# Performance work log

Hardware: AMD Instinct MI355X
Metric: run time of the kernel (lower is better)

## Reference

```python
import jax, jax.numpy as jnp
import numpy as np

L, B, T, C, H, D, F, W = 2, 2, 2048, 1024, 16, 64, 4096, 256
NEG = -1e9
EPS = 1e-6


def _rms(x, g):
    return x * jax.lax.rsqrt(jnp.mean(x * x, axis=-1, keepdims=True) + EPS) * g


def setup_inputs() -> dict:
    key = jax.random.key(0)
    ks = jax.random.split(key, 12)
    s = 0.02
    return {
        "x": jax.random.normal(ks[0], (B, T, C), jnp.float32),
        "retrieval_context": jax.random.normal(ks[1], (B, C), jnp.float32),
        "norm1_g": jnp.ones((L, C), jnp.float32),
        "Wqkv": jax.random.normal(ks[2], (L, C, 3 * C), jnp.float32) * s,
        "Wproj": jax.random.normal(ks[3], (L, C, C), jnp.float32) * s,
        "gate_W": jax.random.normal(ks[4], (L, C, 3), jnp.float32) * 0.01,
        "gate_b": jnp.zeros((L, 3), jnp.float32),
        "ret_W": jax.random.normal(ks[5], (L, C, C), jnp.float32) * 0.01,
        "norm2_g": jnp.ones((L, C), jnp.float32),
        "ffn_gate_W": jax.random.normal(ks[6], (L, C, F), jnp.float32) * s,
        "ffn_up_W": jax.random.normal(ks[7], (L, C, F), jnp.float32) * s,
        "ffn_down_W": jax.random.normal(ks[8], (L, F, C), jnp.float32) * s,
    }


def reference(x, retrieval_context, norm1_g, Wqkv, Wproj, gate_W, gate_b, ret_W,
              norm2_g, ffn_gate_W, ffn_up_W, ffn_down_W):
    # Sliding-window causal mask: key j visible to query i iff i-W+1 <= j <= i
    pos = jnp.arange(T)
    allowed = (pos[None, :] <= pos[:, None]) & (pos[None, :] >= pos[:, None] - W + 1)
    mask = jnp.where(allowed, 0.0, NEG).astype(x.dtype)  # (T, T)
    scale = 1.0 / np.sqrt(D)

    for l in range(L):
        h = _rms(x, norm1_g[l])                              # (B,T,C)
        qkv = h @ Wqkv[l]                                    # (B,T,3C)
        q, k, v = jnp.split(qkv, 3, axis=-1)
        q = q.reshape(B, T, H, D).transpose(0, 2, 1, 3)       # (B,H,T,D)
        k = k.reshape(B, T, H, D).transpose(0, 2, 1, 3)
        v = v.reshape(B, T, H, D).transpose(0, 2, 1, 3)
        scores = jnp.einsum("bhqd,bhkd->bhqk", q, k) * scale + mask
        attn = jax.nn.softmax(scores, axis=-1)
        o = jnp.einsum("bhqk,bhkd->bhqd", attn, v)
        attn_out = o.transpose(0, 2, 1, 3).reshape(B, T, C) @ Wproj[l]

        # TRN disabled: trn_out == 0, gate channel 1 pinned to -1e9
        gate_logits = h @ gate_W[l] + gate_b[l]               # (B,T,3)
        gate_logits = gate_logits.at[..., 1].set(NEG)
        gates = jax.nn.softmax(gate_logits, axis=-1)

        ret_out = (retrieval_context @ ret_W[l])[:, None, :]   # (B,1,C) broadcast over T
        mixed = gates[..., 0:1] * attn_out + gates[..., 2:3] * ret_out
        x = x + mixed

        h2 = _rms(x, norm2_g[l])
        ffn = (jax.nn.silu(h2 @ ffn_gate_W[l]) * (h2 @ ffn_up_W[l])) @ ffn_down_W[l]
        x = x + ffn
    return x
```

## Files before the change

### kernel.cpp

```cpp
#include <hip/hip_runtime.h>

#define L_ 2
#define B_ 2
#define T_ 2048
#define C_ 1024
#define H_ 16
#define D_ 64
#define F_ 4096
#define NTOK 4096
#define NELEM 4194304

typedef unsigned short u16;
typedef __attribute__((ext_vector_type(8))) short short8;
typedef __attribute__((ext_vector_type(4))) float float4v;

__device__ __forceinline__ float bf2f(u16 u) {
  unsigned v = ((unsigned)u) << 16;
  return __builtin_bit_cast(float, v);
}
__device__ __forceinline__ u16 f2bf(float f) {
  unsigned u = __builtin_bit_cast(unsigned, f);
  u += 0x7FFFu + ((u >> 16) & 1u);
  return (u16)(u >> 16);
}

__global__ void k_copyf(const float* __restrict__ in, float* __restrict__ out) {
  const int i = blockIdx.x * 256 + threadIdx.x;
  out[i] = in[i];
}

__device__ __forceinline__ void rms_tail(float* vloc, const float* __restrict__ g,
                                         u16* __restrict__ orow) {
  float s = vloc[0] * vloc[0] + vloc[1] * vloc[1] + vloc[2] * vloc[2] + vloc[3] * vloc[3];
#pragma unroll
  for (int o = 32; o; o >>= 1) s += __shfl_down(s, o);
  __shared__ float red[4];
  __shared__ float rsv;
  if ((threadIdx.x & 63) == 0) red[threadIdx.x >> 6] = s;
  __syncthreads();
  if (threadIdx.x == 0) {
    float t = red[0] + red[1] + red[2] + red[3];
    rsv = rsqrtf(t * (1.f / C_) + 1e-6f);
  }
  __syncthreads();
  const float rr = rsv;
#pragma unroll
  for (int i = 0; i < 4; i++) {
    const int c = threadIdx.x + i * 256;
    orow[c] = f2bf(vloc[i] * rr * g[c]);
  }
}

__global__ __launch_bounds__(256) void k_rms_first(const float* __restrict__ xin,
                                                   const float* __restrict__ g,
                                                   float* __restrict__ x,
                                                   u16* __restrict__ out) {
  const int row = blockIdx.x;
  const float* sr = xin + (size_t)row * C_;
  float* xr = x + (size_t)row * C_;
  float vloc[4];
#pragma unroll
  for (int i = 0; i < 4; i++) {
    const int c = threadIdx.x + i * 256;
    const float v = sr[c];
    vloc[i] = v;
    xr[c] = v;
  }
  rms_tail(vloc, g, out + (size_t)row * C_);
}

__global__ __launch_bounds__(256) void k_rms(const float* __restrict__ x,
                                             const float* __restrict__ g,
                                             u16* __restrict__ out) {
  const int row = blockIdx.x;
  const float* xr = x + (size_t)row * C_;
  float vloc[4];
#pragma unroll
  for (int i = 0; i < 4; i++) vloc[i] = xr[threadIdx.x + i * 256];
  rms_tail(vloc, g, out + (size_t)row * C_);
}

__global__ __launch_bounds__(256) void k_rms2mix(float* __restrict__ x,
                                                 const float* __restrict__ gates,
                                                 const float* __restrict__ ret,
                                                 const float* __restrict__ g,
                                                 u16* __restrict__ out) {
  const int row = blockIdx.x;
  const int b = row >> 11;
  const float g2 = gates[row * 2 + 1];
  const float* rr_ = ret + b * C_;
  float* xr = x + (size_t)row * C_;
  float vloc[4];
#pragma unroll
  for (int i = 0; i < 4; i++) {
    const int c = threadIdx.x + i * 256;
    const float v = xr[c] + g2 * rr_[c];
    vloc[i] = v;
    xr[c] = v;
  }
  rms_tail(vloc, g, out + (size_t)row * C_);
}

__global__ void k_tr2(const float* __restrict__ s0, u16* __restrict__ d0,
                      int K0, int N0, int t0,
                      const float* __restrict__ s1, u16* __restrict__ d1,
                      int K1, int N1) {
  __shared__ float tile[32][33];
  int t = blockIdx.x;
  const float* src; u16* dst; int K, N;
  if (t < t0) { src = s0; dst = d0; K = K0; N = N0; }
  else { t -= t0; src = s1; dst = d1; K = K1; N = N1; }
  const int ntx = N >> 5;
  const int tx = t % ntx, ty = t / ntx;
  const int x = tx * 32 + threadIdx.x;
  const int y0 = ty * 32 + threadIdx.y;
#pragma unroll
  for (int i = 0; i < 32; i += 8) tile[threadIdx.y + i][threadIdx.x] = src[(size_t)(y0 + i) * N + x];
  __syncthreads();
  const int x2 = ty * 32 + threadIdx.x;
  const int y2 = tx * 32 + threadIdx.y;
#pragma unroll
  for (int i = 0; i < 32; i += 8) dst[(size_t)(y2 + i) * K + x2] = f2bf(tile[threadIdx.x][threadIdx.y + i]);
}

__global__ void k_tr1(const float* __restrict__ in, u16* __restrict__ out, int K, int N) {
  __shared__ float tile[32][33];
  const int ntx = N >> 5;
  const int tx = blockIdx.x % ntx, ty = blockIdx.x / ntx;
  const int x = tx * 32 + threadIdx.x;
  const int y0 = ty * 32 + threadIdx.y;
#pragma unroll
  for (int i = 0; i < 32; i += 8) tile[threadIdx.y + i][threadIdx.x] = in[(size_t)(y0 + i) * N + x];
  __syncthreads();
  const int x2 = ty * 32 + threadIdx.x;
  const int y2 = tx * 32 + threadIdx.y;
#pragma unroll
  for (int i = 0; i < 32; i += 8) out[(size_t)(y2 + i) * K + x2] = f2bf(tile[threadIdx.x][threadIdx.y + i]);
}

__global__ void k_vt(const u16* __restrict__ qkv, u16* __restrict__ Vt) {
  __shared__ u16 tile[32][34];
  const int jt = blockIdx.x;
  const int dt = blockIdx.y;
  const int bh = blockIdx.z;
  const int b = bh >> 4;
  const int h = bh & 15;
  const int tx = threadIdx.x, ty = threadIdx.y;
#pragma unroll
  for (int i = 0; i < 32; i += 8) {
    const int j = jt * 32 + ty + i;
    const int d = dt * 32 + tx;
    tile[ty + i][tx] = qkv[(size_t)(b * T_ + j) * (3 * C_) + 2 * C_ + h * D_ + d];
  }
  __syncthreads();
#pragma unroll
  for (int i = 0; i < 32; i += 8) {
    const int d = dt * 32 + ty + i;
    const int j = jt * 32 + tx;
    Vt[(size_t)(bh * D_ + d) * T_ + j] = tile[tx][ty + i];
  }
}


#define VMW(n) asm volatile("s_waitcnt vmcnt(" #n ")" ::: "memory")
#define LGKM0 asm volatile("s_waitcnt lgkmcnt(0)" ::: "memory")
#define GBAR() __builtin_amdgcn_s_barrier()
#define PRIO1() __builtin_amdgcn_s_setprio(1)
#define PRIO0() __builtin_amdgcn_s_setprio(0)

#define STG8(gsrc, grow0, dstbyte, kk)                                                    \
  do {                                                                                    \
    const u16* g0_ = (gsrc) + (size_t)((grow0) + wid * 8 + srow) * K + (kk) + scol;       \
    __builtin_amdgcn_global_load_lds(                                                     \
        (const __attribute__((address_space(1))) void*)g0_,                               \
        (__attribute__((address_space(3))) void*)(lc + (dstbyte) + wid * 8 * 128),        \
        16, 0, 0);                                                                        \
    const u16* g1_ = g0_ + (size_t)64 * K;                                                \
    __builtin_amdgcn_global_load_lds(                                                     \
        (const __attribute__((address_space(1))) void*)g1_,                               \
        (__attribute__((address_space(3))) void*)(lc + (dstbyte) + (64 + wid * 8) * 128), \
        16, 0, 0);                                                                        \
  } while (0)

#define RDA4(dst, bufbyte, ig0)                                                           \
  { _Pragma("unroll") for (int i_ = 0; i_ < 4; ++i_) {                                    \
      _Pragma("unroll") for (int s_ = 0; s_ < 2; ++s_)                                    \
        dst[i_][s_] = *(const short8*)(lc + (bufbyte) +                                   \
            (wm * 128 + ((ig0) + i_) * 16 + m16) * 128 + (((s_ * 4 + quad) ^ csw) * 16)); } }

#define RDB4(dst, bufbyte, jg0)                                                           \
  { _Pragma("unroll") for (int j_ = 0; j_ < 2; ++j_) {                                    \
      _Pragma("unroll") for (int s_ = 0; s_ < 2; ++s_)                                    \
        dst[j_][s_] = *(const short8*)(lc + (bufbyte) +                                   \
            (wn * 64 + ((jg0) + j_) * 16 + m16) * 128 + (((s_ * 4 + quad) ^ csw) * 16)); } }

#define RDBS(dst, bufbyte)                                                                \
  { _Pragma("unroll") for (int j_ = 0; j_ < 2; ++j_) {                                    \
      _Pragma("unroll") for (int s_ = 0; s_ < 2; ++s_)                                    \
        dst[j_][s_] = *(const short8*)(lc + (bufbyte) +                                   \
            (wn * 32 + j_ * 16 + m16) * 128 + (((s_ * 4 + quad) ^ csw) * 16)); } }

#define MM16(ig0, jg0, bv_)                                                               \
  { _Pragma("unroll") for (int i_ = 0; i_ < 4; ++i_) {                                    \
      _Pragma("unroll") for (int j_ = 0; j_ < 2; ++j_) {                                  \
        _Pragma("unroll") for (int s_ = 0; s_ < 2; ++s_)                                  \
          acc[(ig0) + i_][(jg0) + j_] = __builtin_amdgcn_mfma_f32_16x16x32_bf16(          \
              av[i_][s_], bv_[j_][s_], acc[(ig0) + i_][(jg0) + j_], 0, 0, 0); } } }

#define MMS(accv, ig0, bv_)                                                               \
  { _Pragma("unroll") for (int i_ = 0; i_ < 4; ++i_) {                                    \
      _Pragma("unroll") for (int j_ = 0; j_ < 2; ++j_) {                                  \
        _Pragma("unroll") for (int s_ = 0; s_ < 2; ++s_)                                  \
          accv[(ig0) + i_][j_] = __builtin_amdgcn_mfma_f32_16x16x32_bf16(                 \
              av[i_][s_], bv_[j_][s_], accv[(ig0) + i_][j_], 0, 0, 0); } } }

template <int EPI>
__global__ __launch_bounds__(512, 2) void k_g256(const u16* __restrict__ A,
                                                 const u16* __restrict__ Bt,
                                                 u16* __restrict__ Cc,
                                                 float* __restrict__ Xf,
                                                 const float* __restrict__ gates,
                                                 int N, int K) {
  extern __shared__ __align__(16) u16 lds[];
  char* const lc = (char*)lds;
  enum { A0B = 0, B0B = 32768, A1B = 65536, B1B = 98304 };
  const int tid = threadIdx.x;
  const int wid = tid >> 6, lane = tid & 63;
  const int wm = wid >> 2, wn = wid & 3;
  const int quad = lane >> 4, m16 = lane & 15;
  const int srow = lane >> 3, sc = lane & 7;
  const int scol = ((sc ^ srow) & 7) * 8;
  const int csw = m16 & 7;
  const int m0 = blockIdx.x * 256, n0 = blockIdx.y * 256;
  const int Kslice = K / gridDim.z;
  const int kbeg = blockIdx.z * Kslice;
  const int ntile = Kslice >> 6;
  const int nit = ntile >> 1;

  float4v acc[8][4];
#pragma unroll
  for (int i = 0; i < 8; i++)
#pragma unroll
    for (int j = 0; j < 4; j++) acc[i][j] = (float4v){0.f, 0.f, 0.f, 0.f};
  short8 av[4][2], b01[2][2], b23[2][2];

  STG8(Bt, n0, B0B, kbeg);
  STG8(Bt, n0 + 128, B0B + 16384, kbeg);
  STG8(A, m0, A0B, kbeg);
  STG8(A, m0 + 128, A0B + 16384, kbeg);
  STG8(Bt, n0, B1B, kbeg + 64);
  STG8(Bt, n0 + 128, B1B + 16384, kbeg + 64);
  VMW(4);
  GBAR();

#pragma unroll 1
  for (int it = 0; it < nit; ++it) {
    const int t2 = 2 * it + 2, t3 = 2 * it + 3;
    const int k1 = kbeg + (2 * it + 1) * 64;
    const int k2 = kbeg + (t2 < ntile ? t2 : t2 - ntile) * 64;
    const int k3 = kbeg + (t3 < ntile ? t3 : t3 - ntile) * 64;
    RDA4(av, A0B, 0);
    RDB4(b01, B0B, 0);
    STG8(A, m0, A1B, k1);
    GBAR(); LGKM0;
    PRIO1(); MM16(0, 0, b01); PRIO0();
    GBAR();
    RDB4(b23, B0B, 2);
    STG8(A, m0 + 128, A1B + 16384, k1);
    GBAR(); LGKM0;
    PRIO1(); MM16(0, 2, b23); PRIO0();
    GBAR();
    RDA4(av, A0B, 4);
    STG8(Bt, n0, B0B, k2);
    GBAR(); LGKM0;
    PRIO1(); MM16(4, 2, b23); PRIO0();
    GBAR();
    STG8(Bt, n0 + 128, B0B + 16384, k2);
    VMW(4);
    GBAR(); LGKM0;
    PRIO1(); MM16(4, 0, b01); PRIO0();
    GBAR();
    RDA4(av, A1B, 0);
    RDB4(b01, B1B, 0);
    STG8(A, m0, A0B, k2);
    GBAR(); LGKM0;
    PRIO1(); MM16(0, 0, b01); PRIO0();
    GBAR();
    RDB4(b23, B1B, 2);
    STG8(A, m0 + 128, A0B + 16384, k2);
    GBAR(); LGKM0;
    PRIO1(); MM16(0, 2, b23); PRIO0();
    GBAR();
    RDA4(av, A1B, 4);
    STG8(Bt, n0, B1B, k3);
    GBAR(); LGKM0;
    PRIO1(); MM16(4, 2, b23); PRIO0();
    GBAR();
    STG8(Bt, n0 + 128, B1B + 16384, k3);
    VMW(4);
    GBAR(); LGKM0;
    PRIO1(); MM16(4, 0, b01); PRIO0();
    GBAR();
  }

#pragma unroll
  for (int i = 0; i < 8; i++) {
    const int row0 = m0 + wm * 128 + i * 16 + quad * 4;
#pragma unroll
    for (int j = 0; j < 4; j++) {
      const int col = n0 + wn * 64 + j * 16 + m16;
#pragma unroll
      for (int r = 0; r < 4; r++) {
        const size_t idx = (size_t)(row0 + r) * N + col;
        const float v = acc[i][j][r];
        if (EPI == 0) Cc[idx] = f2bf(v);
        else if (EPI == 1) unsafeAtomicAdd(&Xf[idx], gates[(row0 + r) * 2] * v);
        else unsafeAtomicAdd(&Xf[idx], v);
      }
    }
  }
}

__global__ __launch_bounds__(512, 2) void k_g256s(const u16* __restrict__ A,
                                                  const u16* __restrict__ Btg,
                                                  const u16* __restrict__ Btu,
                                                  u16* __restrict__ Cc,
                                                  int N, int K) {
  extern __shared__ __align__(16) u16 lds[];
  char* const lc = (char*)lds;
  enum { SA0 = 0, SG0 = 32768, SU0 = 49152, SA1 = 65536, SG1 = 98304, SU1 = 114688 };
  const int tid = threadIdx.x;
  const int wid = tid >> 6, lane = tid & 63;
  const int wm = wid >> 2, wn = wid & 3;
  const int quad = lane >> 4, m16 = lane & 15;
  const int srow = lane >> 3, sc = lane & 7;
  const int scol = ((sc ^ srow) & 7) * 8;
  const int csw = m16 & 7;
  const int m0 = blockIdx.x * 256, n0 = blockIdx.y * 128;
  const int kbeg = 0;
  const int ntile = K >> 6;
  const int nit = ntile >> 1;

  float4v accg[8][2], accu[8][2];
#pragma unroll
  for (int i = 0; i < 8; i++)
#pragma unroll
    for (int j = 0; j < 2; j++) {
      accg[i][j] = (float4v){0.f, 0.f, 0.f, 0.f};
      accu[i][j] = (float4v){0.f, 0.f, 0.f, 0.f};
    }
  short8 av[4][2], bg[2][2], bu[2][2];

  STG8(Btg, n0, SG0, kbeg);
  STG8(Btu, n0, SU0, kbeg);
  STG8(A, m0, SA0, kbeg);
  STG8(A, m0 + 128, SA0 + 16384, kbeg);
  STG8(Btg, n0, SG1, kbeg + 64);
  STG8(Btu, n0, SU1, kbeg + 64);
  STG8(A, m0, SA1, kbeg + 64);
  VMW(6);
  GBAR();

#pragma unroll 1
  for (int it = 0; it < nit; ++it) {
    const int t2 = 2 * it + 2, t3 = 2 * it + 3;
    const int k1 = kbeg + (2 * it + 1) * 64;
    const int k2 = kbeg + (t2 < ntile ? t2 : t2 - ntile) * 64;
    const int k3 = kbeg + (t3 < ntile ? t3 : t3 - ntile) * 64;
    RDA4(av, SA0, 0);
    RDBS(bg, SG0);
    STG8(A, m0 + 128, SA1 + 16384, k1);
    GBAR(); LGKM0;
    PRIO1(); MMS(accg, 0, bg); PRIO0();
    GBAR();
    RDBS(bu, SU0);
    STG8(Btg, n0, SG0, k2);
    GBAR(); LGKM0;
    PRIO1(); MMS(accu, 0, bu); PRIO0();
    GBAR();
    RDA4(av, SA0, 4);
    STG8(Btu, n0, SU0, k2);
    GBAR(); LGKM0;
    PRIO1(); MMS(accu, 4, bu); PRIO0();
    GBAR();
    STG8(A, m0, SA0, k2);
    VMW(6);
    GBAR(); LGKM0;
    PRIO1(); MMS(accg, 4, bg); PRIO0();
    GBAR();
    RDA4(av, SA1, 0);
    RDBS(bg, SG1);
    STG8(A, m0 + 128, SA0 + 16384, k2);
    GBAR(); LGKM0;
    PRIO1(); MMS(accg, 0, bg); PRIO0();
    GBAR();
    RDBS(bu, SU1);
    STG8(Btg, n0, SG1, k3);
    GBAR(); LGKM0;
    PRIO1(); MMS(accu, 0, bu); PRIO0();
    GBAR();
    RDA4(av, SA1, 4);
    STG8(Btu, n0, SU1, k3);
    GBAR(); LGKM0;
    PRIO1(); MMS(accu, 4, bu); PRIO0();
    GBAR();
    STG8(A, m0, SA1, k3);
    VMW(6);
    GBAR(); LGKM0;
    PRIO1(); MMS(accg, 4, bg); PRIO0();
    GBAR();
  }

#pragma unroll
  for (int i = 0; i < 8; i++) {
    const int row0 = m0 + wm * 128 + i * 16 + quad * 4;
#pragma unroll
    for (int j = 0; j < 2; j++) {
      const int col = n0 + wn * 32 + j * 16 + m16;
#pragma unroll
      for (int r = 0; r < 4; r++) {
        const float g = accg[i][j][r];
        const float u = accu[i][j][r];
        Cc[(size_t)(row0 + r) * N + col] = f2bf(u * g / (1.f + __expf(-g)));
      }
    }
  }
}

__global__ __launch_bounds__(256) void k_attn(const u16* __restrict__ qkv,
                                              const u16* __restrict__ Vt,
                                              u16* __restrict__ o) {
  __shared__ u16 lds[4][16][290];
  const int wave = threadIdx.x >> 6;
  const int widG = blockIdx.x * 4 + wave;
  const int lane = threadIdx.x & 63;
  const int quad = lane >> 4;
  const int c16 = lane & 15;
  const int qt = (widG & 127) * 16;
  const int h = (widG >> 7) & 15;
  const int b = widG >> 11;
  const size_t rs = 3 * C_;
  const int jt0 = qt - 256;

  const u16* qrow = qkv + (size_t)(b * T_ + qt + c16) * rs + h * D_ + quad * 8;
  const short8 a0 = *(const short8*)(qrow);
  const short8 a1 = *(const short8*)(qrow + 32);
  float4v S[17];
  const short8 z8 = (short8){0, 0, 0, 0, 0, 0, 0, 0};
#pragma unroll
  for (int t = 0; t < 17; t++) {
    if (jt0 + t * 16 + 15 < 0) { S[t] = (float4v){0.f, 0.f, 0.f, 0.f}; continue; }
    const int j = jt0 + t * 16 + c16;
    short8 b0 = z8, b1 = z8;
    if (j >= 0) {
      const u16* krow = qkv + (size_t)(b * T_ + j) * rs + C_ + h * D_ + quad * 8;
      b0 = *(const short8*)(krow);
      b1 = *(const short8*)(krow + 32);
    }
    float4v z = (float4v){0.f, 0.f, 0.f, 0.f};
    z = __builtin_amdgcn_mfma_f32_16x16x32_bf16(a0, b0, z, 0, 0, 0);
    z = __builtin_amdgcn_mfma_f32_16x16x32_bf16(a1, b1, z, 0, 0, 0);
    S[t] = z;
  }
#pragma unroll
  for (int r = 0; r < 4; r++) {
    const int q = qt + quad * 4 + r;
    float mx = -1.0e30f;
#pragma unroll
    for (int t = 0; t < 17; t++) {
      const int j = jt0 + t * 16 + c16;
      const int w = j - q + 255;
      const bool vis = (j >= 0) && (w >= 0) && (w < 256);
      if (vis) {
        const float s = S[t][r] * 0.125f;
        S[t][r] = s;
        mx = fmaxf(mx, s);
      } else {
        S[t][r] = -1.0e30f;
      }
    }
#pragma unroll
    for (int o2 = 1; o2 < 16; o2 <<= 1) mx = fmaxf(mx, __shfl_xor(mx, o2));
    float sum = 0.f;
#pragma unroll
    for (int t = 0; t < 17; t++) {
      const float e = (S[t][r] > -0.9e30f) ? __expf(S[t][r] - mx) : 0.f;
      S[t][r] = e;
      sum += e;
    }
#pragma unroll
    for (int o2 = 1; o2 < 16; o2 <<= 1) sum += __shfl_xor(sum, o2);
    const float inv = 1.f / fmaxf(sum, 1e-30f);
    const int prow = quad * 4 + r;
#pragma unroll
    for (int t = 0; t < 17; t++) lds[wave][prow][t * 16 + c16] = f2bf(S[t][r] * inv);
    lds[wave][prow][272 + c16] = 0;
  }
  __syncthreads();

  float4v acc[4];
#pragma unroll
  for (int md = 0; md < 4; md++) acc[md] = (float4v){0.f, 0.f, 0.f, 0.f};
  const u16* vtb = Vt + (size_t)((b * H_ + h) * D_) * T_;
  const uint* prow32 = (const uint*)(&lds[wave][c16][0]);
  union { short8 s8; uint u[4]; } bf;
#pragma unroll
  for (int c = 0; c < 9; c++) {
    const int jbase = jt0 + c * 32;
    if (jbase + 31 < 0) continue;
#pragma unroll
    for (int w2 = 0; w2 < 4; w2++) bf.u[w2] = prow32[c * 16 + quad * 4 + w2];
    int j0 = jbase + quad * 8;
    j0 = (j0 < 0) ? 0 : ((j0 > T_ - 8) ? (T_ - 8) : j0);
#pragma unroll
    for (int md = 0; md < 4; md++) {
      const short8 af = *(const short8*)(vtb + (size_t)(md * 16 + c16) * T_ + j0);
      acc[md] = __builtin_amdgcn_mfma_f32_16x16x32_bf16(af, bf.s8, acc[md], 0, 0, 0);
    }
  }
#pragma unroll
  for (int md = 0; md < 4; md++) {
    uint u0 = (uint)f2bf(acc[md][0]) | ((uint)f2bf(acc[md][1]) << 16);
    uint u1 = (uint)f2bf(acc[md][2]) | ((uint)f2bf(acc[md][3]) << 16);
    uint2 pk = make_uint2(u0, u1);
    u16* dst = o + (size_t)(b * T_ + qt + c16) * C_ + h * D_ + md * 16 + quad * 4;
    *(uint2*)dst = pk;
  }
}

__global__ __launch_bounds__(256) void k_gate(const u16* __restrict__ h,
                                              const float* __restrict__ gW,
                                              const float* __restrict__ gb,
                                              float* __restrict__ gates) {
  const int row = blockIdx.x * 4 + (threadIdx.x >> 6);
  const int lane = threadIdx.x & 63;
  const u16* hr = h + (size_t)row * C_;
  float s0 = 0.f, s2 = 0.f;
  for (int k = lane; k < C_; k += 64) {
    const float hv = bf2f(hr[k]);
    s0 += hv * gW[k * 3 + 0];
    s2 += hv * gW[k * 3 + 2];
  }
#pragma unroll
  for (int o = 32; o; o >>= 1) { s0 += __shfl_down(s0, o); s2 += __shfl_down(s2, o); }
  if (lane == 0) {
    const float l0 = s0 + gb[0];
    const float l2 = s2 + gb[2];
    const float m = fmaxf(l0, l2);
    const float e0 = __expf(l0 - m), e2 = __expf(l2 - m);
    const float inv = 1.f / (e0 + e2);
    gates[row * 2 + 0] = e0 * inv;
    gates[row * 2 + 1] = e2 * inv;
  }
}

__global__ void k_ret2(const float* __restrict__ rc, const float* __restrict__ rW,
                       float* __restrict__ ret) {
  const int l = blockIdx.x >> 3;
  const int bid = blockIdx.x & 7;
  const int b = bid >> 2;
  const int col = (bid & 3) * 256 + threadIdx.x;
  const float* rWl = rW + (size_t)l * C_ * C_;
  float s = 0.f;
  for (int k = 0; k < C_; k++) s += rc[b * C_ + k] * rWl[(size_t)k * C_ + col];
  ret[(size_t)l * B_ * C_ + b * C_ + col] = s;
}

extern "C" void kernel_launch(void* const* d_in, const int* in_sizes, int n_in,
                              void* d_out, int out_size, void* d_ws, size_t ws_size,
                              hipStream_t stream) {
  (void)in_sizes; (void)n_in; (void)out_size; (void)ws_size;
  const float* xin  = (const float*)d_in[0];
  const float* rc   = (const float*)d_in[1];
  const float* n1g  = (const float*)d_in[2];
  const float* Wqkv = (const float*)d_in[3];
  const float* Wpro = (const float*)d_in[4];
  const float* gW   = (const float*)d_in[5];
  const float* gb   = (const float*)d_in[6];
  const float* rW   = (const float*)d_in[7];
  const float* n2g  = (const float*)d_in[8];
  const float* fgW  = (const float*)d_in[9];
  const float* fuW  = (const float*)d_in[10];
  const float* fdW  = (const float*)d_in[11];

  static bool attr_done = false;
  if (!attr_done) {
    hipFuncSetAttribute((const void*)k_g256<0>, hipFuncAttributeMaxDynamicSharedMemorySize, 131072);
    hipFuncSetAttribute((const void*)k_g256<1>, hipFuncAttributeMaxDynamicSharedMemorySize, 131072);
    hipFuncSetAttribute((const void*)k_g256<2>, hipFuncAttributeMaxDynamicSharedMemorySize, 131072);
    hipFuncSetAttribute((const void*)k_g256s, hipFuncAttributeMaxDynamicSharedMemorySize, 131072);
    attr_done = true;
  }

  char* w = (char*)d_ws;
  float* gates = (float*)(w);
  float* retb  = (float*)(w + 32768);
  float* xf32  = (float*)(w + 65536);
  u16* hbuf    = (u16*)(w + 65536 + (size_t)NELEM * 4);
  u16* big     = hbuf + NELEM;
  u16* qkv  = big;
  u16* obuf = big + (size_t)NTOK * 3 * C_;
  u16* gbuf = big;
  u16* wT  = (u16*)d_out;
  u16* wTp = wT + (size_t)3 * C_ * C_;
  u16* Vt  = (u16*)d_out + (size_t)NELEM;
  u16* wT2 = Vt;

  k_ret2<<<16, 256, 0, stream>>>(rc, rW, retb);

  for (int l = 0; l < L_; l++) {
    if (l == 0)
      k_rms_first<<<NTOK, 256, 0, stream>>>(xin, n1g, xf32, hbuf);
    else
      k_rms<<<NTOK, 256, 0, stream>>>(xf32, n1g + l * C_, hbuf);
    k_tr2<<<3072 + 1024, dim3(32, 8), 0, stream>>>(
        Wqkv + (size_t)l * C_ * 3 * C_, wT, C_, 3 * C_, 3072,
        Wpro + (size_t)l * C_ * C_, wTp, C_, C_);
    k_g256<0><<<dim3(NTOK / 256, 3 * C_ / 256, 1), 512, 131072, stream>>>(
        hbuf, wT, qkv, nullptr, nullptr, 3 * C_, C_);
    k_gate<<<NTOK / 4, 256, 0, stream>>>(hbuf, gW + (size_t)l * C_ * 3, gb + l * 3, gates);
    k_vt<<<dim3(64, 2, 32), dim3(32, 8), 0, stream>>>(qkv, Vt);
    k_attn<<<1024, 256, 0, stream>>>(qkv, Vt, obuf);
    k_g256<1><<<dim3(NTOK / 256, C_ / 256, 2), 512, 131072, stream>>>(
        obuf, wTp, nullptr, xf32, gates, C_, C_);
    k_rms2mix<<<NTOK, 256, 0, stream>>>(xf32, gates, retb + (size_t)l * B_ * C_,
                                        n2g + l * C_, hbuf);
    k_tr2<<<4096 + 4096, dim3(32, 8), 0, stream>>>(
        fgW + (size_t)l * C_ * F_, wT, C_, F_, 4096,
        fuW + (size_t)l * C_ * F_, wT2, C_, F_);
    k_g256s<<<dim3(NTOK / 256, F_ / 128, 1), 512, 131072, stream>>>(
        hbuf, wT, wT2, gbuf, F_, C_);
    k_tr1<<<4096, dim3(32, 8), 0, stream>>>(fdW + (size_t)l * F_ * C_, hbuf, F_, C_);
    k_g256<2><<<dim3(NTOK / 256, C_ / 256, 4), 512, 131072, stream>>>(
        gbuf, hbuf, nullptr, xf32, nullptr, C_, F_);
  }

  k_copyf<<<NELEM / 256, 256, 0, stream>>>(xf32, (float*)d_out);
}
```

Measured before the change: 843.6 us.

## Replace atomic split-K GEMMs with 256x128 tiles and a deferred partial-sum buffer

Adds a GEMM variant with 256x128 output tiles and 96KB of LDS, used for the attention output projection and the FFN down projection. The output projection now runs without split-K and applies the gate directly in its epilogue. The FFN down projection uses only two K slices: slice 0 writes its partial sum to a scratch buffer in the output memory, and slice 1 adds into the residual. That scratch partial is folded into the residual by the next layer's RMS-norm kernel or by the final copy. The goal is to remove contended read-modify-write traffic on the residual. The cost is an extra fp32 buffer pass, and the scratch buffer's reuse of output memory that also holds transposed weights depends on launch order.

```diff
diff --git a/kernel.cpp b/kernel.cpp
--- a/kernel.cpp
+++ b/kernel.cpp
@@ -24,9 +24,9 @@
   return (u16)(u >> 16);
 }
 
-__global__ void k_copyf(const float* __restrict__ in, float* __restrict__ out) {
+__global__ void k_copyf_acc(const float* __restrict__ in, float* __restrict__ out) {
   const int i = blockIdx.x * 256 + threadIdx.x;
-  out[i] = in[i];
+  out[i] = in[i] + out[i];
 }
 
 __device__ __forceinline__ void rms_tail(float* vloc, const float* __restrict__ g,
@@ -69,14 +69,21 @@
   rms_tail(vloc, g, out + (size_t)row * C_);
 }
 
-__global__ __launch_bounds__(256) void k_rms(const float* __restrict__ x,
-                                             const float* __restrict__ g,
-                                             u16* __restrict__ out) {
+__global__ __launch_bounds__(256) void k_rms_acc(float* __restrict__ x,
+                                                 const float* __restrict__ pf,
+                                                 const float* __restrict__ g,
+                                                 u16* __restrict__ out) {
   const int row = blockIdx.x;
-  const float* xr = x + (size_t)row * C_;
+  float* xr = x + (size_t)row * C_;
+  const float* pr = pf + (size_t)row * C_;
   float vloc[4];
 #pragma unroll
-  for (int i = 0; i < 4; i++) vloc[i] = xr[threadIdx.x + i * 256];
+  for (int i = 0; i < 4; i++) {
+    const int c = threadIdx.x + i * 256;
+    const float v = xr[c] + pr[c];
+    vloc[i] = v;
+    xr[c] = v;
+  }
   rms_tail(vloc, g, out + (size_t)row * C_);
 }
 
@@ -161,7 +168,6 @@
   }
 }
 
-
 #define VMW(n) asm volatile("s_waitcnt vmcnt(" #n ")" ::: "memory")
 #define LGKM0 asm volatile("s_waitcnt lgkmcnt(0)" ::: "memory")
 #define GBAR() __builtin_amdgcn_s_barrier()
@@ -213,6 +219,13 @@
         _Pragma("unroll") for (int s_ = 0; s_ < 2; ++s_)                                  \
           accv[(ig0) + i_][j_] = __builtin_amdgcn_mfma_f32_16x16x32_bf16(                 \
               av[i_][s_], bv_[j_][s_], accv[(ig0) + i_][j_], 0, 0, 0); } } }
+
+#define MMN(ig0, bv_)                                                                     \
+  { _Pragma("unroll") for (int i_ = 0; i_ < 4; ++i_) {                                    \
+      _Pragma("unroll") for (int j_ = 0; j_ < 2; ++j_) {                                  \
+        _Pragma("unroll") for (int s_ = 0; s_ < 2; ++s_)                                  \
+          acc[(ig0) + i_][j_] = __builtin_amdgcn_mfma_f32_16x16x32_bf16(                  \
+              av8[(ig0) + i_][s_], bv_[j_][s_], acc[(ig0) + i_][j_], 0, 0, 0); } } }
 
 template <int EPI>
 __global__ __launch_bounds__(512, 2) void k_g256(const u16* __restrict__ A,
@@ -321,6 +334,99 @@
   }
 }
 
+template <int EPI>
+__global__ __launch_bounds__(512, 2) void k_g256n(const u16* __restrict__ A,
+                                                  const u16* __restrict__ Bt,
+                                                  float* __restrict__ Xf,
+                                                  float* __restrict__ Pf,
+                                                  const float* __restrict__ gates,
+                                                  int N, int K) {
+  extern __shared__ __align__(16) u16 lds[];
+  char* const lc = (char*)lds;
+  enum { SA0 = 0, SB0 = 32768, SA1 = 49152, SB1 = 81920 };
+  const int tid = threadIdx.x;
+  const int wid = tid >> 6, lane = tid & 63;
+  const int wm = wid >> 2, wn = wid & 3;
+  const int quad = lane >> 4, m16 = lane & 15;
+  const int srow = lane >> 3, sc = lane & 7;
+  const int scol = ((sc ^ srow) & 7) * 8;
+  const int csw = m16 & 7;
+  const int m0 = blockIdx.x * 256, n0 = blockIdx.y * 128;
+  const int Kslice = K / gridDim.z;
+  const int kbeg = blockIdx.z * Kslice;
+  const int ntile = Kslice >> 6;
+  const int nit = ntile >> 1;
+
+  float4v acc[8][2];
+#pragma unroll
+  for (int i = 0; i < 8; i++)
+#pragma unroll
+    for (int j = 0; j < 2; j++) acc[i][j] = (float4v){0.f, 0.f, 0.f, 0.f};
+  short8 av8[8][2], bv[2][2];
+
+  STG8(Bt, n0, SB0, kbeg);
+  STG8(A, m0, SA0, kbeg);
+  STG8(A, m0 + 128, SA0 + 16384, kbeg);
+  STG8(Bt, n0, SB1, kbeg + 64);
+  STG8(A, m0, SA1, kbeg + 64);
+  STG8(A, m0 + 128, SA1 + 16384, kbeg + 64);
+  VMW(6);
+  GBAR();
+
+#pragma unroll 1
+  for (int it = 0; it < nit; ++it) {
+    const int t2 = 2 * it + 2, t3 = 2 * it + 3;
+    const int k2 = kbeg + (t2 < ntile ? t2 : t2 - ntile) * 64;
+    const int k3 = kbeg + (t3 < ntile ? t3 : t3 - ntile) * 64;
+    RDA4(av8, SA0, 0);
+    RDA4((&av8[4]), SA0, 4);
+    RDBS(bv, SB0);
+    GBAR(); LGKM0;
+    PRIO1(); MMN(0, bv); PRIO0();
+    GBAR();
+    STG8(Bt, n0, SB0, k2);
+    STG8(A, m0, SA0, k2);
+    STG8(A, m0 + 128, SA0 + 16384, k2);
+    VMW(6);
+    GBAR(); LGKM0;
+    PRIO1(); MMN(4, bv); PRIO0();
+    GBAR();
+    RDA4(av8, SA1, 0);
+    RDA4((&av8[4]), SA1, 4);
+    RDBS(bv, SB1);
+    GBAR(); LGKM0;
+    PRIO1(); MMN(0, bv); PRIO0();
+    GBAR();
+    STG8(Bt, n0, SB1, k3);
+    STG8(A, m0, SA1, k3);
+    STG8(A, m0 + 128, SA1 + 16384, k3);
+    VMW(6);
+    GBAR(); LGKM0;
+    PRIO1(); MMN(4, bv); PRIO0();
+    GBAR();
+  }
+
+#pragma unroll
+  for (int i = 0; i < 8; i++) {
+    const int row0 = m0 + wm * 128 + i * 16 + quad * 4;
+#pragma unroll
+    for (int j = 0; j < 2; j++) {
+      const int col = n0 + wn * 32 + j * 16 + m16;
+#pragma unroll
+      for (int r = 0; r < 4; r++) {
+        const size_t idx = (size_t)(row0 + r) * N + col;
+        const float v = acc[i][j][r];
+        if (EPI == 1) {
+          Xf[idx] += gates[(row0 + r) * 2] * v;
+        } else {
+          if (blockIdx.z == 0) Pf[idx] = v;
+          else Xf[idx] += v;
+        }
+      }
+    }
+  }
+}
+
 __global__ __launch_bounds__(512, 2) void k_g256s(const u16* __restrict__ A,
                                                   const u16* __restrict__ Btg,
                                                   const u16* __restrict__ Btu,
@@ -340,6 +446,8 @@
   const int kbeg = 0;
   const int ntile = K >> 6;
   const int nit = ntile >> 1;
+  const int K2 = K;
+  (void)K2;
 
   float4v accg[8][2], accu[8][2];
 #pragma unroll
@@ -586,9 +694,9 @@
   static bool attr_done = false;
   if (!attr_done) {
     hipFuncSetAttribute((const void*)k_g256<0>, hipFuncAttributeMaxDynamicSharedMemorySize, 131072);
-    hipFuncSetAttribute((const void*)k_g256<1>, hipFuncAttributeMaxDynamicSharedMemorySize, 131072);
-    hipFuncSetAttribute((const void*)k_g256<2>, hipFuncAttributeMaxDynamicSharedMemorySize, 131072);
     hipFuncSetAttribute((const void*)k_g256s, hipFuncAttributeMaxDynamicSharedMemorySize, 131072);
+    hipFuncSetAttribute((const void*)k_g256n<1>, hipFuncAttributeMaxDynamicSharedMemorySize, 98304);
+    hipFuncSetAttribute((const void*)k_g256n<2>, hipFuncAttributeMaxDynamicSharedMemorySize, 98304);
     attr_done = true;
   }
 
@@ -605,6 +713,7 @@
   u16* wTp = wT + (size_t)3 * C_ * C_;
   u16* Vt  = (u16*)d_out + (size_t)NELEM;
   u16* wT2 = Vt;
+  float* Pf = (float*)d_out;
 
   k_ret2<<<16, 256, 0, stream>>>(rc, rW, retb);
 
@@ -612,7 +721,7 @@
     if (l == 0)
       k_rms_first<<<NTOK, 256, 0, stream>>>(xin, n1g, xf32, hbuf);
     else
-      k_rms<<<NTOK, 256, 0, stream>>>(xf32, n1g + l * C_, hbuf);
+      k_rms_acc<<<NTOK, 256, 0, stream>>>(xf32, Pf, n1g + l * C_, hbuf);
     k_tr2<<<3072 + 1024, dim3(32, 8), 0, stream>>>(
         Wqkv + (size_t)l * C_ * 3 * C_, wT, C_, 3 * C_, 3072,
         Wpro + (size_t)l * C_ * C_, wTp, C_, C_);
@@ -621,8 +730,8 @@
     k_gate<<<NTOK / 4, 256, 0, stream>>>(hbuf, gW + (size_t)l * C_ * 3, gb + l * 3, gates);
     k_vt<<<dim3(64, 2, 32), dim3(32, 8), 0, stream>>>(qkv, Vt);
     k_attn<<<1024, 256, 0, stream>>>(qkv, Vt, obuf);
-    k_g256<1><<<dim3(NTOK / 256, C_ / 256, 2), 512, 131072, stream>>>(
-        obuf, wTp, nullptr, xf32, gates, C_, C_);
+    k_g256n<1><<<dim3(NTOK / 256, C_ / 128, 1), 512, 98304, stream>>>(
+        obuf, wTp, xf32, nullptr, gates, C_, C_);
     k_rms2mix<<<NTOK, 256, 0, stream>>>(xf32, gates, retb + (size_t)l * B_ * C_,
                                         n2g + l * C_, hbuf);
     k_tr2<<<4096 + 4096, dim3(32, 8), 0, stream>>>(
@@ -631,9 +740,9 @@
     k_g256s<<<dim3(NTOK / 256, F_ / 128, 1), 512, 131072, stream>>>(
         hbuf, wT, wT2, gbuf, F_, C_);
     k_tr1<<<4096, dim3(32, 8), 0, stream>>>(fdW + (size_t)l * F_ * C_, hbuf, F_, C_);
-    k_g256<2><<<dim3(NTOK / 256, C_ / 256, 4), 512, 131072, stream>>>(
-        gbuf, hbuf, nullptr, xf32, nullptr, C_, F_);
-  }
-
-  k_copyf<<<NELEM / 256, 256, 0, stream>>>(xf32, (float*)d_out);
-}
+    k_g256n<2><<<dim3(NTOK / 256, C_ / 128, 2), 512, 98304, stream>>>(
+        gbuf, hbuf, xf32, Pf, nullptr, C_, F_);
+  }
+
+  k_copyf_acc<<<NELEM / 256, 256, 0, stream>>>(xf32, (float*)d_out);
+}
```

Result: faster. 822.6 us (-2.5%).
